# Optimization experiments

Hardware: AMD Instinct MI355X
Metric: run time of the kernel (lower is better)

## Reference

```python
import jax, jax.numpy as jnp
import numpy as np

V, D, MAXLEN, B, C = 32000, 1024, 2048, 4, 2048


def setup_inputs() -> dict:
    key = jax.random.key(0)
    ks = jax.random.split(key, 8)
    x = jax.random.randint(ks[0], (B, C), 0, V, dtype=jnp.int64)
    s = 0.02
    embed = jax.random.normal(ks[1], (V, D), dtype=jnp.float32) * s
    pe = jax.random.normal(ks[2], (MAXLEN, D), dtype=jnp.float32) * s
    Wq = jax.random.normal(ks[3], (D, D), dtype=jnp.float32) * s
    Wk = jax.random.normal(ks[4], (D, D), dtype=jnp.float32) * s
    Wv = jax.random.normal(ks[5], (D, D), dtype=jnp.float32) * s
    Wo = jax.random.normal(ks[6], (V, D), dtype=jnp.float32) * s
    bo = jnp.zeros((V,), dtype=jnp.float32)
    return {"x": x, "embed": embed, "pe": pe, "Wq": Wq, "Wk": Wk, "Wv": Wv, "Wo": Wo, "bo": bo}


def reference(x, embed, pe, Wq, Wk, Wv, Wo, bo):
    Bc, Cc = x.shape
    Dd = embed.shape[1]
    # token embedding + learned absolute PE (pos_offset = 0)
    h = embed[x] + pe[:Cc]                      # (B, C, D)
    # single-head Q/K/V projections (torch Linear: y = x @ W.T)
    Q = jnp.einsum('bcd,ed->bce', h, Wq)
    K = jnp.einsum('bcd,ed->bce', h, Wk)
    Vv = jnp.einsum('bcd,ed->bce', h, Wv)
    scores = jnp.einsum('bqd,bkd->bqk', Q, K) / jnp.sqrt(jnp.float32(Dd))
    # additive causal mask: 0 on lower triangle, -inf above
    mask = jnp.where(jnp.tril(jnp.ones((Cc, Cc), dtype=bool)), 0.0, -jnp.inf).astype(scores.dtype)
    weights = jax.nn.softmax(scores + mask, axis=-1)  # (B, C, C)
    attn_out = jnp.einsum('bqk,bkd->bqd', weights, Vv)
    hidden = h + attn_out
    logits = jnp.einsum('bcd,vd->bcv', hidden, Wo) + bo
    return logits
```

## Files before the change

### kernel.cpp

```cpp
#include <hip/hip_runtime.h>

#define DEV __device__ __forceinline__

typedef __attribute__((ext_vector_type(8))) __bf16 bf16x8;
typedef __attribute__((ext_vector_type(4))) float f32x4;

DEV unsigned short f2bf(float f) {
    unsigned u = __builtin_bit_cast(unsigned, f);
    u += 0x7fffu + ((u >> 16) & 1u);
    return (unsigned short)(u >> 16);
}
DEV float bf2f(unsigned short s) {
    unsigned u = ((unsigned)s) << 16;
    return __builtin_bit_cast(float, u);
}

DEV void gload_lds16(const unsigned short* g, unsigned short* l) {
    __builtin_amdgcn_global_load_lds(
        (const __attribute__((address_space(1))) unsigned int*)g,
        (__attribute__((address_space(3))) unsigned int*)l, 16, 0, 0);
}


__global__ __launch_bounds__(256) void k_cast_bf16(const float* __restrict__ src,
                                                   unsigned short* __restrict__ dst, int n4) {
    int i = blockIdx.x * 256 + threadIdx.x;
    if (i >= n4) return;
    float4 v = reinterpret_cast<const float4*>(src)[i];
    ushort4 o;
    o.x = f2bf(v.x); o.y = f2bf(v.y); o.z = f2bf(v.z); o.w = f2bf(v.w);
    reinterpret_cast<ushort4*>(dst)[i] = o;
}

__global__ __launch_bounds__(256) void k_cast3(const float* __restrict__ a,
                                               const float* __restrict__ b,
                                               const float* __restrict__ c,
                                               unsigned short* __restrict__ oa,
                                               unsigned short* __restrict__ ob,
                                               unsigned short* __restrict__ oc,
                                               int n4each) {
    int i = blockIdx.x * 256 + threadIdx.x;
    int w = i / n4each, j = i - w * n4each;
    const float* s = (w == 0) ? a : (w == 1) ? b : c;
    unsigned short* d = (w == 0) ? oa : (w == 1) ? ob : oc;
    float4 v = reinterpret_cast<const float4*>(s)[j];
    ushort4 o;
    o.x = f2bf(v.x); o.y = f2bf(v.y); o.z = f2bf(v.z); o.w = f2bf(v.w);
    reinterpret_cast<ushort4*>(d)[j] = o;
}

__global__ __launch_bounds__(256) void k_prep_h(const int* __restrict__ x,
                                                const float* __restrict__ embed,
                                                const float* __restrict__ pe,
                                                unsigned short* __restrict__ h) {
    const int r = blockIdx.x;
    const int pos = r & 2047;
    const int tok = x[r];
    const int t = threadIdx.x;
    float4 e = reinterpret_cast<const float4*>(embed + (size_t)tok * 1024)[t];
    float4 p = reinterpret_cast<const float4*>(pe + (size_t)pos * 1024)[t];
    ushort4 o;
    o.x = f2bf(e.x + p.x); o.y = f2bf(e.y + p.y);
    o.z = f2bf(e.z + p.z); o.w = f2bf(e.w + p.w);
    reinterpret_cast<ushort4*>(h + (size_t)r * 1024)[t] = o;
}

__global__ __launch_bounds__(256) void k_softmax_causal(const float* __restrict__ S,
                                                        unsigned short* __restrict__ W) {
    const int r = blockIdx.x;
    const int q = r & 2047;
    const float* row = S + (size_t)r * 2048;
    unsigned short* orow = W + (size_t)r * 2048;
    const int t = threadIdx.x;
    const float scale = 0.03125f;
    const int kceil4 = (((q >> 7) + 1) << 7) >> 2;
    float p[8];
    float mx = -1e30f;
    #pragma unroll
    for (int i = 0; i < 2; ++i) {
        int i4 = t + i * 256;
        int base = i4 * 4;
        float4 v = (float4){0.f, 0.f, 0.f, 0.f};
        if (base <= q) v = reinterpret_cast<const float4*>(row)[i4];
        p[i*4+0] = (base+0 <= q) ? v.x * scale : -1e30f;
        p[i*4+1] = (base+1 <= q) ? v.y * scale : -1e30f;
        p[i*4+2] = (base+2 <= q) ? v.z * scale : -1e30f;
        p[i*4+3] = (base+3 <= q) ? v.w * scale : -1e30f;
        #pragma unroll
        for (int j = 0; j < 4; ++j) mx = fmaxf(mx, p[i*4+j]);
    }
    #pragma unroll
    for (int o = 32; o > 0; o >>= 1) mx = fmaxf(mx, __shfl_xor(mx, o));
    __shared__ float redm[4];
    __shared__ float reds[4];
    const int w = t >> 6;
    if ((t & 63) == 0) redm[w] = mx;
    __syncthreads();
    mx = fmaxf(fmaxf(redm[0], redm[1]), fmaxf(redm[2], redm[3]));
    float e[8];
    float s = 0.f;
    #pragma unroll
    for (int i = 0; i < 8; ++i) { e[i] = __expf(p[i] - mx); s += e[i]; }
    #pragma unroll
    for (int o = 32; o > 0; o >>= 1) s += __shfl_xor(s, o);
    if ((t & 63) == 0) reds[w] = s;
    __syncthreads();
    s = (reds[0] + reds[1]) + (reds[2] + reds[3]);
    const float inv = 1.0f / s;
    #pragma unroll
    for (int i = 0; i < 2; ++i) {
        int i4 = t + i * 256;
        if (i4 < kceil4) {
            ushort4 o4;
            o4.x = f2bf(e[i*4+0] * inv);
            o4.y = f2bf(e[i*4+1] * inv);
            o4.z = f2bf(e[i*4+2] * inv);
            o4.w = f2bf(e[i*4+3] * inv);
            reinterpret_cast<ushort4*>(orow)[i4] = o4;
        }
    }
}

template<int OUT_BF16, int TRANS_OUT, int ADD_BIAS, int ADD_RES, int CAUSAL_SKIP, int TRI_K>
__global__ __launch_bounds__(256)
void k_gemm_bt(const unsigned short* __restrict__ A,
               const unsigned short* __restrict__ B,
               void* __restrict__ Out,
               const float* __restrict__ bias,
               const unsigned short* __restrict__ Res,
               int M, int N, int K, int ldo,
               long long sA, long long sB, long long sC, long long sRes) {
    const int bm = blockIdx.x, bn = blockIdx.y, bz = blockIdx.z;
    if (CAUSAL_SKIP && bn > bm) return;
    A += (long long)bz * sA;
    B += (long long)bz * sB;

    __shared__ __align__(16) unsigned short As[128 * 32];
    __shared__ __align__(16) unsigned short Bs[128 * 32];

    const int t = threadIdx.x;
    const int w = t >> 6;
    const int lane = t & 63;
    const int wm = w >> 1, wn = w & 1;
    const int fr = lane & 15, fq = lane >> 4;

    f32x4 acc[4][4];
    #pragma unroll
    for (int mi = 0; mi < 4; ++mi)
        #pragma unroll
        for (int ni = 0; ni < 4; ++ni)
            acc[mi][ni] = (f32x4){0.f, 0.f, 0.f, 0.f};

    const int kend = TRI_K ? ((K < (bm + 1) * 128) ? K : (bm + 1) * 128) : K;

    const int c0 = t, c1 = t + 256;
    const unsigned short* gA0 = A + (size_t)(bm * 128 + (c0 >> 2)) * K + (c0 & 3) * 8;
    const unsigned short* gA1 = A + (size_t)(bm * 128 + (c1 >> 2)) * K + (c1 & 3) * 8;
    const unsigned short* gB0 = B + (size_t)(bn * 128 + (c0 >> 2)) * K + (c0 & 3) * 8;
    const unsigned short* gB1 = B + (size_t)(bn * 128 + (c1 >> 2)) * K + (c1 & 3) * 8;
    unsigned short* lA0 = As + w * 512;
    unsigned short* lA1 = As + 2048 + w * 512;
    unsigned short* lB0 = Bs + w * 512;
    unsigned short* lB1 = Bs + 2048 + w * 512;

    for (int kt = 0; kt < kend; kt += 32) {
        gload_lds16(gA0 + kt, lA0);
        gload_lds16(gA1 + kt, lA1);
        gload_lds16(gB0 + kt, lB0);
        gload_lds16(gB1 + kt, lB1);
        __syncthreads();

        bf16x8 af[4], bfr[4];
        #pragma unroll
        for (int mi = 0; mi < 4; ++mi)
            af[mi] = *reinterpret_cast<const bf16x8*>(As + (wm * 64 + mi * 16 + fr) * 32 + fq * 8);
        #pragma unroll
        for (int ni = 0; ni < 4; ++ni)
            bfr[ni] = *reinterpret_cast<const bf16x8*>(Bs + (wn * 64 + ni * 16 + fr) * 32 + fq * 8);
        #pragma unroll
        for (int mi = 0; mi < 4; ++mi)
            #pragma unroll
            for (int ni = 0; ni < 4; ++ni)
                acc[mi][ni] = __builtin_amdgcn_mfma_f32_16x16x32_bf16(af[mi], bfr[ni], acc[mi][ni], 0, 0, 0);
        __syncthreads();
    }

    const int row0 = bm * 128 + wm * 64 + fq * 4;
    const int col0 = bn * 128 + wn * 64 + fr;
    if (OUT_BF16) {
        unsigned short* O = (unsigned short*)Out + (long long)bz * sC;
        #pragma unroll
        for (int mi = 0; mi < 4; ++mi) {
            #pragma unroll
            for (int j = 0; j < 4; ++j) {
                const int row = row0 + mi * 16 + j;
                unsigned short* orow = O + (size_t)row * ldo;
                const unsigned short* rrow =
                    ADD_RES ? (Res + (long long)bz * sRes + (size_t)row * ldo) : (const unsigned short*)nullptr;
                #pragma unroll
                for (int ni = 0; ni < 4; ++ni) {
                    const int col = col0 + ni * 16;
                    float v = acc[mi][ni][j];
                    if (ADD_RES) v += bf2f(rrow[col]);
                    orow[col] = f2bf(v);
                }
            }
        }
    } else {
        float* O = (float*)Out + (long long)bz * sC;
        #pragma unroll
        for (int mi = 0; mi < 4; ++mi) {
            #pragma unroll
            for (int j = 0; j < 4; ++j) {
                const int row = row0 + mi * 16 + j;
                float* orow = O + (size_t)row * ldo;
                #pragma unroll
                for (int ni = 0; ni < 4; ++ni) {
                    const int col = col0 + ni * 16;
                    float v = acc[mi][ni][j];
                    if (ADD_BIAS) v += bias[col];
                    orow[col] = v;
                }
            }
        }
    }
}


#define SA3(buf, kt) do { \
    unsigned short* d_ = Lds + (buf)*16384 + w*512; \
    gload_lds16(gA0 + (kt)*32, d_); \
    gload_lds16(gA1 + (kt)*32, d_ + 4096); } while(0)

#define SB3(buf, kt) do { \
    unsigned short* d_ = Lds + (buf)*16384 + 8192 + w*512; \
    gload_lds16(gB0 + (kt)*32, d_); \
    gload_lds16(gB1 + (kt)*32, d_ + 4096); } while(0)

#define LDA3(buf, mi) (*reinterpret_cast<const bf16x8*>(Lds + (buf)*16384 + aBase + (mi)*512))
#define LDB3(buf, ni) (*reinterpret_cast<const bf16x8*>(Lds + (buf)*16384 + 8192 + bBase + (ni)*512))

#define MF16(arow, af) do { \
    __builtin_amdgcn_s_setprio(1); \
    _Pragma("unroll") \
    for (int j_ = 0; j_ < 4; ++j_) \
        _Pragma("unroll") \
        for (int n_ = 0; n_ < 4; ++n_) \
            acc[(arow)+j_][n_] = __builtin_amdgcn_mfma_f32_16x16x32_bf16(af[j_], bb[n_], acc[(arow)+j_][n_], 0, 0, 0); \
    __builtin_amdgcn_s_setprio(0); } while(0)

#define BARX asm volatile("s_barrier" ::: "memory")

template<int EPI>
__global__ __launch_bounds__(512, 2)
void k_g256(const unsigned short* __restrict__ A,
            const unsigned short* __restrict__ B,
            void* __restrict__ O0, void* __restrict__ O1, void* __restrict__ O2,
            const float* __restrict__ bias) {
    constexpr int K = 1024;
    __shared__ __align__(16) unsigned short Lds[49152];

    int bm, bn, bz = 0;
    if (EPI == 2) {
        bm = blockIdx.x; bn = blockIdx.y; bz = blockIdx.z;
        if (bn > bm) return;
    } else if (EPI == 1) {
        int wg = blockIdx.x;
        wg = (wg & 7) * 48 + (wg >> 3);
        bm = wg % 32; bn = wg / 32;
    } else {
        int wg = blockIdx.x;
        wg = (wg & 7) * 500 + (wg >> 3);
        const int tb = wg / 20, u = wg % 20;
        bm = (tb & 7) * 4 + (u & 3);
        bn = (tb >> 3) * 5 + (u >> 2);
    }

    const unsigned short* Ab = A + (EPI == 2 ? (size_t)bz * 2048 * K : 0);
    const unsigned short* Bb2 = B + (EPI == 2 ? (size_t)bz * 2048 * K : 0);

    const int tid = threadIdx.x;
    const int w = tid >> 6, lane = tid & 63;
    const int wm = w >> 2, wn = w & 3;
    const int fr = lane & 15, fq = lane >> 4;
    const int sl = fq ^ ((fr >> 1) & 3);

    const int c0 = w * 64 + lane, c1 = c0 + 512;
    const int r0 = c0 >> 2, s0 = ((c0 & 3) ^ ((r0 >> 1) & 3)) * 8;
    const int r1 = c1 >> 2, s1 = ((c1 & 3) ^ ((r1 >> 1) & 3)) * 8;
    const unsigned short* gA0 = Ab + (size_t)(bm * 256 + r0) * K + s0;
    const unsigned short* gA1 = Ab + (size_t)(bm * 256 + r1) * K + s1;
    const unsigned short* gB0 = Bb2 + (size_t)(bn * 256 + r0) * K + s0;
    const unsigned short* gB1 = Bb2 + (size_t)(bn * 256 + r1) * K + s1;

    const int aBase = (wm * 128 + fr) * 32 + sl * 8;
    const int bBase = (wn * 64 + fr) * 32 + sl * 8;

    f32x4 acc[8][4];
    #pragma unroll
    for (int i = 0; i < 8; ++i)
        #pragma unroll
        for (int j = 0; j < 4; ++j)
            acc[i][j] = (f32x4){0.f, 0.f, 0.f, 0.f};

    SA3(0, 0); SB3(0, 0);
    SA3(1, 1); SB3(1, 1);
    asm volatile("s_waitcnt vmcnt(4)" ::: "memory");
    BARX;
    bf16x8 a0[4], bb[4];
    #pragma unroll
    for (int j = 0; j < 4; ++j) a0[j] = LDA3(0, j);
    #pragma unroll
    for (int j = 0; j < 4; ++j) bb[j] = LDB3(0, j);

    #pragma unroll
    for (int t = 0; t < 32; ++t) {
        const int bc = t % 3, b1 = (t + 1) % 3, bs = (t + 2) % 3;
        const int ks = (t + 2) & 31;
        bf16x8 a1t[4];
        #pragma unroll
        for (int j = 0; j < 4; ++j) a1t[j] = LDA3(bc, 4 + j);
        SA3(bs, ks);
        BARX;
        MF16(0, a0);
        asm volatile("s_waitcnt vmcnt(2)" ::: "memory");
        BARX;
        bf16x8 a0n[4], bn_[4];
        #pragma unroll
        for (int j = 0; j < 4; ++j) a0n[j] = LDA3(b1, j);
        #pragma unroll
        for (int j = 0; j < 4; ++j) bn_[j] = LDB3(b1, j);
        SB3(bs, ks);
        BARX;
        MF16(4, a1t);
        BARX;
        #pragma unroll
        for (int j = 0; j < 4; ++j) { a0[j] = a0n[j]; bb[j] = bn_[j]; }
    }
    asm volatile("s_waitcnt vmcnt(0)" ::: "memory");

    const int row0 = bm * 256 + wm * 128 + fq * 4;
    const int col0 = bn * 256 + wn * 64 + fr;
    if (EPI == 0) {
        float* Out = (float*)O0;
        float bia[4];
        #pragma unroll
        for (int ni = 0; ni < 4; ++ni) bia[ni] = bias[col0 + ni * 16];
        #pragma unroll
        for (int mi = 0; mi < 8; ++mi) {
            #pragma unroll
            for (int j = 0; j < 4; ++j) {
                float* orow = Out + (size_t)(row0 + mi * 16 + j) * 32000;
                #pragma unroll
                for (int ni = 0; ni < 4; ++ni)
                    orow[col0 + ni * 16] = acc[mi][ni][j] + bia[ni];
            }
        }
    } else if (EPI == 1) {
        if (bn < 8) {
            unsigned short* O = (unsigned short*)(bn < 4 ? O0 : O1);
            const int cb = (bn < 4) ? 0 : 1024;
            #pragma unroll
            for (int mi = 0; mi < 8; ++mi) {
                #pragma unroll
                for (int j = 0; j < 4; ++j) {
                    unsigned short* orow = O + (size_t)(row0 + mi * 16 + j) * 1024;
                    #pragma unroll
                    for (int ni = 0; ni < 4; ++ni)
                        orow[col0 + ni * 16 - cb] = f2bf(acc[mi][ni][j]);
                }
            }
        } else {
            unsigned short* O = (unsigned short*)O2 + (size_t)(row0 >> 11) * 2097152;
            const int i0 = row0 & 2047;
            #pragma unroll
            for (int mi = 0; mi < 8; ++mi) {
                #pragma unroll
                for (int ni = 0; ni < 4; ++ni) {
                    const int e = col0 + ni * 16 - 2048;
                    ushort4 o4;
                    o4.x = f2bf(acc[mi][ni][0]);
                    o4.y = f2bf(acc[mi][ni][1]);
                    o4.z = f2bf(acc[mi][ni][2]);
                    o4.w = f2bf(acc[mi][ni][3]);
                    *reinterpret_cast<ushort4*>(O + (size_t)e * 2048 + i0 + mi * 16) = o4;
                }
            }
        }
    } else {
        float* Out = (float*)O0 + (size_t)bz * 2048 * 2048;
        #pragma unroll
        for (int mi = 0; mi < 8; ++mi) {
            #pragma unroll
            for (int j = 0; j < 4; ++j) {
                float* orow = Out + (size_t)(row0 + mi * 16 + j) * 2048;
                #pragma unroll
                for (int ni = 0; ni < 4; ++ni)
                    orow[col0 + ni * 16] = acc[mi][ni][j];
            }
        }
    }
}


extern "C" void kernel_launch(void* const* d_in, const int* in_sizes, int n_in,
                              void* d_out, int out_size, void* d_ws, size_t ws_size,
                              hipStream_t stream) {
    (void)in_sizes; (void)n_in; (void)out_size; (void)ws_size;
    constexpr int Bb = 4, Cc = 2048, Dd = 1024, Vv = 32000;
    constexpr int M = Bb * Cc;

    const int*   x     = (const int*)d_in[0];
    const float* embed = (const float*)d_in[1];
    const float* pe    = (const float*)d_in[2];
    const float* Wq    = (const float*)d_in[3];
    const float* Wk    = (const float*)d_in[4];
    const float* Wv    = (const float*)d_in[5];
    const float* Wo    = (const float*)d_in[6];
    const float* bo    = (const float*)d_in[7];
    float* out = (float*)d_out;

    char* p = (char*)d_ws;
    auto au = [&](size_t n) { unsigned short* r = (unsigned short*)p; p += n * sizeof(unsigned short); return r; };
    unsigned short* h_bf   = au((size_t)M * Dd);
    unsigned short* hid_bf = au((size_t)M * Dd);
    unsigned short* Qb     = au((size_t)M * Dd);
    unsigned short* Kb     = au((size_t)M * Dd);
    unsigned short* Vt     = au((size_t)M * Dd);
    unsigned short* Wqb    = au((size_t)Dd * Dd);
    unsigned short* Wkb    = au((size_t)Dd * Dd);
    unsigned short* Wvb    = au((size_t)Dd * Dd);
    unsigned short* Wob    = au((size_t)Vv * Dd);
    unsigned short* Wt     = au((size_t)Bb * Cc * Cc);
    float* Sc = (float*)p;

    k_cast3<<<dim3(3 * Dd * Dd / 4 / 256), 256, 0, stream>>>(Wq, Wk, Wv, Wqb, Wkb, Wvb, Dd * Dd / 4);
    k_cast_bf16<<<dim3(Vv * Dd / 4 / 256), 256, 0, stream>>>(Wo, Wob, Vv * Dd / 4);
    k_prep_h<<<dim3(M), 256, 0, stream>>>(x, embed, pe, h_bf);

    k_g256<1><<<dim3(384), 512, 0, stream>>>(h_bf, Wqb, Qb, Kb, Vt, nullptr);

    k_g256<2><<<dim3(8, 8, 4), 512, 0, stream>>>(Qb, Kb, Sc, nullptr, nullptr, nullptr);

    k_softmax_causal<<<dim3(M), 256, 0, stream>>>(Sc, Wt);

    {
        dim3 g(Cc / 128, Dd / 128, Bb);
        k_gemm_bt<1,0,0,1,0,1><<<g, 256, 0, stream>>>(Wt, Vt, hid_bf, nullptr, h_bf,
            Cc, Dd, Cc, Dd, (long long)Cc * Cc, (long long)Dd * Cc, (long long)Cc * Dd, (long long)Cc * Dd);
    }

    k_g256<0><<<dim3(4000), 512, 0, stream>>>(hid_bf, Wob, out, nullptr, nullptr, bo);
}
```

Before: 793.2 us.

## Replace logits GEMM with 128x256-tile kernel using triple-buffered LDS pipeline

The output-projection GEMM (8192x32000x1024) moves from the shared 256x256-tile k_g256 kernel to a dedicated k_glog kernel. It uses 128x256 tiles, a smaller LDS footprint with a 3-stage global_load_lds ring, and launch bounds allowing 4 blocks per CU. Blocks are remapped so each XCD works on a band of M tiles. The goal is higher occupancy and better latency hiding for the largest GEMM, which writes the fp32 logits. In exchange, A/B reuse per tile drops and the grid doubles to 8000 blocks.

```diff
diff --git a/kernel.cpp b/kernel.cpp
--- a/kernel.cpp
+++ b/kernel.cpp
@@ -264,16 +264,10 @@
     if (EPI == 2) {
         bm = blockIdx.x; bn = blockIdx.y; bz = blockIdx.z;
         if (bn > bm) return;
-    } else if (EPI == 1) {
+    } else {
         int wg = blockIdx.x;
         wg = (wg & 7) * 48 + (wg >> 3);
         bm = wg % 32; bn = wg / 32;
-    } else {
-        int wg = blockIdx.x;
-        wg = (wg & 7) * 500 + (wg >> 3);
-        const int tb = wg / 20, u = wg % 20;
-        bm = (tb & 7) * 4 + (u & 3);
-        bn = (tb >> 3) * 5 + (u >> 2);
     }
 
     const unsigned short* Ab = A + (EPI == 2 ? (size_t)bz * 2048 * K : 0);
@@ -341,22 +335,7 @@
 
     const int row0 = bm * 256 + wm * 128 + fq * 4;
     const int col0 = bn * 256 + wn * 64 + fr;
-    if (EPI == 0) {
-        float* Out = (float*)O0;
-        float bia[4];
-        #pragma unroll
-        for (int ni = 0; ni < 4; ++ni) bia[ni] = bias[col0 + ni * 16];
-        #pragma unroll
-        for (int mi = 0; mi < 8; ++mi) {
-            #pragma unroll
-            for (int j = 0; j < 4; ++j) {
-                float* orow = Out + (size_t)(row0 + mi * 16 + j) * 32000;
-                #pragma unroll
-                for (int ni = 0; ni < 4; ++ni)
-                    orow[col0 + ni * 16] = acc[mi][ni][j] + bia[ni];
-            }
-        }
-    } else if (EPI == 1) {
+    if (EPI == 1) {
         if (bn < 8) {
             unsigned short* O = (unsigned short*)(bn < 4 ? O0 : O1);
             const int cb = (bn < 4) ? 0 : 1024;
@@ -400,6 +379,104 @@
             }
         }
     }
+}
+
+
+__global__ __launch_bounds__(512, 4)
+void k_glog(const unsigned short* __restrict__ A,
+            const unsigned short* __restrict__ B,
+            float* __restrict__ Out,
+            const float* __restrict__ bias) {
+    constexpr int K = 1024;
+    __shared__ __align__(16) unsigned short Lds[36864];
+
+    const int wg = blockIdx.x;
+    const int xcd = wg & 7;
+    const int idx = wg >> 3;
+    const int tn = idx / 40;
+    const int u  = idx % 40;
+    const int bm = xcd * 8 + (u & 7);
+    const int bn = tn * 5 + (u >> 3);
+
+    const int tid = threadIdx.x;
+    const int w = tid >> 6, lane = tid & 63;
+    const int wm = w >> 2, wn = w & 3;
+    const int fr = lane & 15, fq = lane >> 4;
+    const int sl = fq ^ ((fr >> 1) & 3);
+
+    const int rA = tid >> 2;
+    const int sA = ((tid & 3) ^ ((rA >> 1) & 3)) * 8;
+    const unsigned short* gA  = A + (size_t)(bm * 128 + rA) * K + sA;
+    const unsigned short* gB0 = B + (size_t)(bn * 256 + rA) * K + sA;
+    const unsigned short* gB1 = B + (size_t)(bn * 256 + 128 + rA) * K + sA;
+
+    unsigned short* ldA  = Lds + w * 512;
+    unsigned short* ldB0 = Lds + 12288 + w * 512;
+    unsigned short* ldB1 = Lds + 12288 + 4096 + w * 512;
+
+    const int aOff = (wm * 64 + fr) * 32 + sl * 8;
+    const int bOff = 12288 + (wn * 64 + fr) * 32 + sl * 8;
+
+    f32x4 acc[4][4];
+    #pragma unroll
+    for (int i = 0; i < 4; ++i)
+        #pragma unroll
+        for (int j = 0; j < 4; ++j)
+            acc[i][j] = (f32x4){0.f, 0.f, 0.f, 0.f};
+
+    gload_lds16(gA,      ldA);
+    gload_lds16(gB0,     ldB0);
+    gload_lds16(gB1,     ldB1);
+    gload_lds16(gA  + 32, ldA  + 4096);
+    gload_lds16(gB0 + 32, ldB0 + 8192);
+    gload_lds16(gB1 + 32, ldB1 + 8192);
+    asm volatile("s_waitcnt vmcnt(3)" ::: "memory");
+    BARX;
+
+    #pragma unroll
+    for (int t = 0; t < 32; ++t) {
+        const int buf = t % 3, bs = (t + 2) % 3;
+        if (t <= 29) {
+            gload_lds16(gA  + (t + 2) * 32, ldA  + bs * 4096);
+            gload_lds16(gB0 + (t + 2) * 32, ldB0 + bs * 8192);
+            gload_lds16(gB1 + (t + 2) * 32, ldB1 + bs * 8192);
+        }
+        bf16x8 af[4], bf[4];
+        #pragma unroll
+        for (int mi = 0; mi < 4; ++mi)
+            af[mi] = *reinterpret_cast<const bf16x8*>(Lds + buf * 4096 + aOff + mi * 512);
+        #pragma unroll
+        for (int ni = 0; ni < 4; ++ni)
+            bf[ni] = *reinterpret_cast<const bf16x8*>(Lds + buf * 8192 + bOff + ni * 512);
+        #pragma unroll
+        for (int mi = 0; mi < 4; ++mi)
+            #pragma unroll
+            for (int ni = 0; ni < 4; ++ni)
+                acc[mi][ni] = __builtin_amdgcn_mfma_f32_16x16x32_bf16(af[mi], bf[ni], acc[mi][ni], 0, 0, 0);
+        if (t <= 29) {
+            asm volatile("s_waitcnt vmcnt(3)" ::: "memory");
+        } else if (t == 30) {
+            asm volatile("s_waitcnt vmcnt(0)" ::: "memory");
+        }
+        BARX;
+    }
+
+    const int row0 = bm * 128 + wm * 64 + fq * 4;
+    const int col0 = bn * 256 + wn * 64 + fr;
+    float bia[4];
+    #pragma unroll
+    for (int ni = 0; ni < 4; ++ni) bia[ni] = bias[col0 + ni * 16];
+    #pragma unroll
+    for (int mi = 0; mi < 4; ++mi) {
+        #pragma unroll
+        for (int j = 0; j < 4; ++j) {
+            float* orow = Out + (size_t)(row0 + mi * 16 + j) * 32000;
+            #pragma unroll
+            for (int ni = 0; ni < 4; ++ni)
+                orow[col0 + ni * 16] = acc[mi][ni][j] + bia[ni];
+        }
+    }
+    asm volatile("s_waitcnt vmcnt(0)" ::: "memory");
 }
 
 
@@ -450,5 +527,5 @@
             Cc, Dd, Cc, Dd, (long long)Cc * Cc, (long long)Dd * Cc, (long long)Cc * Dd, (long long)Cc * Dd);
     }
 
-    k_g256<0><<<dim3(4000), 512, 0, stream>>>(hid_bf, Wob, out, nullptr, nullptr, bo);
-}
+    k_glog<<<dim3(8000), 512, 0, stream>>>(hid_bf, Wob, out, bo);
+}
```

Result: slower. 891.2 us (+12.4%).
